# Kernel optimization log

Hardware: AMD Instinct MI355X
Metric: run time of the kernel (lower is better)

## Reference

```python
import jax, jax.numpy as jnp
import numpy as np

B, N, M = 1024, 1024, 64


def setup_inputs() -> dict:
    key = jax.random.key(0)
    ks = jax.random.split(key, 9)
    return {
        "memory": jax.random.normal(ks[0], (B, N, M), dtype=jnp.float32),
        "k": jax.random.normal(ks[1], (B, M), dtype=jnp.float32),
        "beta": jax.random.uniform(ks[2], (B, 1), dtype=jnp.float32),
        "g": jax.random.uniform(ks[3], (B, 1), dtype=jnp.float32),
        "s": jax.random.uniform(ks[4], (B, 3), dtype=jnp.float32),
        "gamma": jax.random.uniform(ks[5], (B, 1), dtype=jnp.float32),
        "w_prev": jax.random.uniform(ks[6], (B, N), dtype=jnp.float32),
        "e": jax.random.uniform(ks[7], (B, M), dtype=jnp.float32),
        "a": jax.random.normal(ks[8], (B, M), dtype=jnp.float32),
    }


def reference(memory, k, beta, g, s, gamma, w_prev, e, a):
    EPS = 1e-16
    COS_EPS = 1e-8  # torch cosine_similarity norm clamp

    # --- _similarity: content addressing (cosine sim + softmax over N) ---
    mem_e = memory + EPS                      # (B, N, M)
    k_e = (k + EPS)[:, None, :]               # (B, 1, M)
    dot = jnp.sum(mem_e * k_e, axis=-1)       # (B, N)
    denom = (jnp.maximum(jnp.linalg.norm(mem_e, axis=-1), COS_EPS)
             * jnp.maximum(jnp.linalg.norm(k_e, axis=-1), COS_EPS))
    wc = jax.nn.softmax(beta * (dot / denom), axis=1)  # (B, N)

    # --- _interpolate ---
    wg = g * wc + (1.0 - g) * w_prev           # (B, N)

    # --- _shift: 3-tap circular convolution, vectorized over batch ---
    # c[i] = s[0]*w[i-1] + s[1]*w[i] + s[2]*w[i+1]  (circular)
    w_hat = (s[:, 0:1] * jnp.roll(wg, 1, axis=1)
             + s[:, 1:2] * wg
             + s[:, 2:3] * jnp.roll(wg, -1, axis=1))

    # --- _sharpen ---
    w = w_hat ** gamma
    w = w / (jnp.sum(w, axis=1, keepdims=True) + EPS)  # (B, N)

    # --- read ---
    read = jnp.einsum('bn,bnm->bm', w, memory)         # (B, M)

    # --- write: rank-1 erase / add ---
    erase = w[:, :, None] * e[:, None, :]              # (B, N, M)
    add = w[:, :, None] * a[:, None, :]                # (B, N, M)
    new_mem = memory * (1.0 - erase) + add             # (B, N, M)

    # pack read (as an extra row) with the updated memory: (B, N+1, M)
    return jnp.concatenate([read[:, None, :], new_mem], axis=1)
```

## Files before the change

### kernel.cpp

```cpp
#include <hip/hip_runtime.h>
#include <cmath>

#define NB 1024
#define NN 1024
#define MM 64
#define NT 512
#define NW (NT / 64)
#define ITS (NN / 32)

typedef float f32x4 __attribute__((ext_vector_type(4)));

__device__ __forceinline__ float block_sum(float v, float* s_tmp) {
    #pragma unroll
    for (int off = 32; off > 0; off >>= 1) v += __shfl_xor(v, off, 64);
    if ((threadIdx.x & 63) == 0) s_tmp[threadIdx.x >> 6] = v;
    __syncthreads();
    float r = 0.0f;
    #pragma unroll
    for (int i = 0; i < NW; ++i) r += s_tmp[i];
    __syncthreads();
    return r;
}

__device__ __forceinline__ float block_max(float v, float* s_tmp) {
    #pragma unroll
    for (int off = 32; off > 0; off >>= 1) v = fmaxf(v, __shfl_xor(v, off, 64));
    if ((threadIdx.x & 63) == 0) s_tmp[threadIdx.x >> 6] = v;
    __syncthreads();
    float r = s_tmp[0];
    #pragma unroll
    for (int i = 1; i < NW; ++i) r = fmaxf(r, s_tmp[i]);
    __syncthreads();
    return r;
}

__global__ void __launch_bounds__(NT, 2) ntm_fused(
    const float* __restrict__ memory,
    const float* __restrict__ k,
    const float* __restrict__ beta,
    const float* __restrict__ g,
    const float* __restrict__ s,
    const float* __restrict__ gamma,
    const float* __restrict__ w_prev,
    const float* __restrict__ e,
    const float* __restrict__ a,
    float* __restrict__ out)
{
    __shared__ float  s_sc[NN];
    __shared__ float  s_w[NN];
    __shared__ float  s_k[MM];
    __shared__ float  s_tmp[NW];
    __shared__ f32x4  s_red[NW * 16];

    const int t  = threadIdx.x;
    const int cg = t & 15;
    const int rg = t >> 4;
    const int b  = blockIdx.x;

    const float* memb = memory + (size_t)b * NN * MM;
    float*       outb = out    + (size_t)b * (NN + 1) * MM;

    const float bet = beta[b], gb = g[b];
    const float s0 = s[b * 3 + 0], s1 = s[b * 3 + 1], s2 = s[b * 3 + 2];
    const float gam = gamma[b];
    const float wp0 = w_prev[(size_t)b * NN + t];
    const float wp1 = w_prev[(size_t)b * NN + t + 512];
    const f32x4 e4 = *(const f32x4*)(e + b * MM + 4 * cg);
    const f32x4 a4 = *(const f32x4*)(a + b * MM + 4 * cg);

    f32x4 mc[ITS];
    #pragma unroll
    for (int it = 0; it < ITS; ++it) {
        int n = it * 32 + rg;
        mc[it] = __builtin_nontemporal_load(
            (const f32x4*)(memb + (size_t)n * MM + 4 * cg));
    }

    if (t < MM) s_k[t] = k[b * MM + t] + 1e-16f;
    float kq = (t < MM) ? s_k[t] * s_k[t] : 0.0f;
    float kden = fmaxf(sqrtf(block_sum(kq, s_tmp)), 1e-8f);
    const f32x4 k4 = ((const f32x4*)s_k)[cg];

    #pragma unroll
    for (int it = 0; it < ITS; ++it) {
        int n = it * 32 + rg;
        f32x4 m4 = mc[it];
        float ex = m4.x + 1e-16f, ey = m4.y + 1e-16f;
        float ez = m4.z + 1e-16f, ew = m4.w + 1e-16f;
        float d = ex * k4.x + ey * k4.y + ez * k4.z + ew * k4.w;
        float q = ex * ex + ey * ey + ez * ez + ew * ew;
        #pragma unroll
        for (int off = 8; off > 0; off >>= 1) {
            d += __shfl_xor(d, off, 64);
            q += __shfl_xor(q, off, 64);
        }
        if (cg == 0) s_sc[n] = bet * d / (fmaxf(sqrtf(q), 1e-8f) * kden);
    }
    __syncthreads();

    float sc0 = s_sc[t], sc1 = s_sc[t + 512];
    float mx = block_max(fmaxf(sc0, sc1), s_tmp);
    float e0 = __expf(sc0 - mx), e1 = __expf(sc1 - mx);
    float inv = 1.0f / block_sum(e0 + e1, s_tmp);

    const float omg = 1.0f - gb;
    s_sc[t]       = gb * e0 * inv + omg * wp0;
    s_sc[t + 512] = gb * e1 * inv + omg * wp1;
    __syncthreads();

    float wv0, wv1;
    {
        int nm = (t == 0) ? NN - 1 : t - 1;
        wv0 = powf(s0 * s_sc[nm] + s1 * s_sc[t] + s2 * s_sc[t + 1], gam);
    }
    {
        int n = t + 512;
        int np = (n == NN - 1) ? 0 : n + 1;
        wv1 = powf(s0 * s_sc[n - 1] + s1 * s_sc[n] + s2 * s_sc[np], gam);
    }
    float winv = 1.0f / (block_sum(wv0 + wv1, s_tmp) + 1e-16f);
    s_w[t]       = wv0 * winv;
    s_w[t + 512] = wv1 * winv;
    __syncthreads();

    f32x4 acc = {0.f, 0.f, 0.f, 0.f};
    #pragma unroll
    for (int it = 0; it < ITS; ++it) {
        int n = it * 32 + rg;
        f32x4 m4 = mc[it];
        float wn = s_w[n];
        acc.x += wn * m4.x; acc.y += wn * m4.y;
        acc.z += wn * m4.z; acc.w += wn * m4.w;
        f32x4 o;
        o.x = m4.x * (1.0f - wn * e4.x) + wn * a4.x;
        o.y = m4.y * (1.0f - wn * e4.y) + wn * a4.y;
        o.z = m4.z * (1.0f - wn * e4.z) + wn * a4.z;
        o.w = m4.w * (1.0f - wn * e4.w) + wn * a4.w;
        __builtin_nontemporal_store(o, (f32x4*)(outb + (size_t)(n + 1) * MM + 4 * cg));
    }

    const int wid = t >> 6, lane = t & 63;
    #pragma unroll
    for (int off = 16; off <= 32; off <<= 1) {
        acc.x += __shfl_xor(acc.x, off, 64);
        acc.y += __shfl_xor(acc.y, off, 64);
        acc.z += __shfl_xor(acc.z, off, 64);
        acc.w += __shfl_xor(acc.w, off, 64);
    }
    if (lane < 16) s_red[wid * 16 + lane] = acc;
    __syncthreads();
    if (t < 16) {
        f32x4 r = {0.f, 0.f, 0.f, 0.f};
        #pragma unroll
        for (int wv = 0; wv < NW; ++wv) {
            f32x4 v = s_red[wv * 16 + t];
            r.x += v.x; r.y += v.y; r.z += v.z; r.w += v.w;
        }
        __builtin_nontemporal_store(r, (f32x4*)(outb + 4 * t));
    }
}

extern "C" void kernel_launch(void* const* d_in, const int* in_sizes, int n_in,
                              void* d_out, int out_size, void* d_ws, size_t ws_size,
                              hipStream_t stream) {
    ntm_fused<<<NB, NT, 0, stream>>>(
        (const float*)d_in[0],
        (const float*)d_in[1],
        (const float*)d_in[2],
        (const float*)d_in[3],
        (const float*)d_in[4],
        (const float*)d_in[5],
        (const float*)d_in[6],
        (const float*)d_in[7],
        (const float*)d_in[8],
        (float*)d_out);
}
```

Baseline: 471.5 us.

## Make kernel persistent over batches with register prefetch of next memory tile

Launches 256 blocks that each process four batch items in sequence. While the current item's updated memory is being stored, the next item's memory slice is loaded into the same registers. The intent is to hide load latency behind the write phase and cut per-block launch overhead. In exchange, fewer blocks are resident, so there is less cross-block overlap during the serial softmax and sharpen reductions.

```diff
diff --git a/kernel.cpp b/kernel.cpp
--- a/kernel.cpp
+++ b/kernel.cpp
@@ -1,12 +1,14 @@
 #include <hip/hip_runtime.h>
 #include <cmath>
 
-#define NB 1024
-#define NN 1024
-#define MM 64
-#define NT 512
-#define NW (NT / 64)
-#define ITS (NN / 32)
+#define NB   1024
+#define NN   1024
+#define MM   64
+#define NT   512
+#define NW   (NT / 64)
+#define ITS  (NN / 32)
+#define GRID 256
+#define BPB  (NB / GRID)
 
 typedef float f32x4 __attribute__((ext_vector_type(4)));
 
@@ -52,118 +54,130 @@
     __shared__ float  s_tmp[NW];
     __shared__ f32x4  s_red[NW * 16];
 
-    const int t  = threadIdx.x;
-    const int cg = t & 15;
-    const int rg = t >> 4;
-    const int b  = blockIdx.x;
-
-    const float* memb = memory + (size_t)b * NN * MM;
-    float*       outb = out    + (size_t)b * (NN + 1) * MM;
-
-    const float bet = beta[b], gb = g[b];
-    const float s0 = s[b * 3 + 0], s1 = s[b * 3 + 1], s2 = s[b * 3 + 2];
-    const float gam = gamma[b];
-    const float wp0 = w_prev[(size_t)b * NN + t];
-    const float wp1 = w_prev[(size_t)b * NN + t + 512];
-    const f32x4 e4 = *(const f32x4*)(e + b * MM + 4 * cg);
-    const f32x4 a4 = *(const f32x4*)(a + b * MM + 4 * cg);
+    const int t    = threadIdx.x;
+    const int cg   = t & 15;
+    const int rg   = t >> 4;
+    const int wid  = t >> 6;
+    const int lane = t & 63;
+    const int coff = 4 * cg;
 
     f32x4 mc[ITS];
-    #pragma unroll
-    for (int it = 0; it < ITS; ++it) {
-        int n = it * 32 + rg;
-        mc[it] = __builtin_nontemporal_load(
-            (const f32x4*)(memb + (size_t)n * MM + 4 * cg));
+    const int bbase = blockIdx.x * BPB;
+
+    {
+        const float* memb = memory + (size_t)bbase * NN * MM;
+        #pragma unroll
+        for (int it = 0; it < ITS; ++it)
+            mc[it] = __builtin_nontemporal_load(
+                (const f32x4*)(memb + (size_t)(it * 32 + rg) * MM + coff));
     }
 
-    if (t < MM) s_k[t] = k[b * MM + t] + 1e-16f;
-    float kq = (t < MM) ? s_k[t] * s_k[t] : 0.0f;
-    float kden = fmaxf(sqrtf(block_sum(kq, s_tmp)), 1e-8f);
-    const f32x4 k4 = ((const f32x4*)s_k)[cg];
+    for (int bi = 0; bi < BPB; ++bi) {
+        const int  b  = bbase + bi;
+        const bool pf = (bi + 1 < BPB);
+        const float* membn = memory + (size_t)(b + 1) * NN * MM;
+        float*       outb  = out    + (size_t)b * (NN + 1) * MM;
 
-    #pragma unroll
-    for (int it = 0; it < ITS; ++it) {
-        int n = it * 32 + rg;
-        f32x4 m4 = mc[it];
-        float ex = m4.x + 1e-16f, ey = m4.y + 1e-16f;
-        float ez = m4.z + 1e-16f, ew = m4.w + 1e-16f;
-        float d = ex * k4.x + ey * k4.y + ez * k4.z + ew * k4.w;
-        float q = ex * ex + ey * ey + ez * ez + ew * ew;
+        const float bet = beta[b], gb = g[b];
+        const float s0 = s[b * 3 + 0], s1 = s[b * 3 + 1], s2 = s[b * 3 + 2];
+        const float gam = gamma[b];
+        const float wp0 = w_prev[(size_t)b * NN + t];
+        const float wp1 = w_prev[(size_t)b * NN + t + 512];
+        const f32x4 e4 = *(const f32x4*)(e + b * MM + coff);
+        const f32x4 a4 = *(const f32x4*)(a + b * MM + coff);
+
+        if (t < MM) s_k[t] = k[b * MM + t] + 1e-16f;
+        float kq = (t < MM) ? s_k[t] * s_k[t] : 0.0f;
+        float kden = fmaxf(sqrtf(block_sum(kq, s_tmp)), 1e-8f);
+        const f32x4 k4 = ((const f32x4*)s_k)[cg];
+
         #pragma unroll
-        for (int off = 8; off > 0; off >>= 1) {
-            d += __shfl_xor(d, off, 64);
-            q += __shfl_xor(q, off, 64);
+        for (int it = 0; it < ITS; ++it) {
+            int n = it * 32 + rg;
+            f32x4 m4 = mc[it];
+            float ex = m4.x + 1e-16f, ey = m4.y + 1e-16f;
+            float ez = m4.z + 1e-16f, ew = m4.w + 1e-16f;
+            float d = ex * k4.x + ey * k4.y + ez * k4.z + ew * k4.w;
+            float q = ex * ex + ey * ey + ez * ez + ew * ew;
+            #pragma unroll
+            for (int off = 8; off > 0; off >>= 1) {
+                d += __shfl_xor(d, off, 64);
+                q += __shfl_xor(q, off, 64);
+            }
+            if (cg == 0) s_sc[n] = bet * d / (fmaxf(sqrtf(q), 1e-8f) * kden);
         }
-        if (cg == 0) s_sc[n] = bet * d / (fmaxf(sqrtf(q), 1e-8f) * kden);
-    }
-    __syncthreads();
+        __syncthreads();
 
-    float sc0 = s_sc[t], sc1 = s_sc[t + 512];
-    float mx = block_max(fmaxf(sc0, sc1), s_tmp);
-    float e0 = __expf(sc0 - mx), e1 = __expf(sc1 - mx);
-    float inv = 1.0f / block_sum(e0 + e1, s_tmp);
+        float sc0 = s_sc[t], sc1 = s_sc[t + 512];
+        float mx = block_max(fmaxf(sc0, sc1), s_tmp);
+        float e0 = __expf(sc0 - mx), e1 = __expf(sc1 - mx);
+        float inv = 1.0f / block_sum(e0 + e1, s_tmp);
 
-    const float omg = 1.0f - gb;
-    s_sc[t]       = gb * e0 * inv + omg * wp0;
-    s_sc[t + 512] = gb * e1 * inv + omg * wp1;
-    __syncthreads();
+        const float omg = 1.0f - gb;
+        s_sc[t]       = gb * e0 * inv + omg * wp0;
+        s_sc[t + 512] = gb * e1 * inv + omg * wp1;
+        __syncthreads();
 
-    float wv0, wv1;
-    {
-        int nm = (t == 0) ? NN - 1 : t - 1;
-        wv0 = powf(s0 * s_sc[nm] + s1 * s_sc[t] + s2 * s_sc[t + 1], gam);
-    }
-    {
-        int n = t + 512;
-        int np = (n == NN - 1) ? 0 : n + 1;
-        wv1 = powf(s0 * s_sc[n - 1] + s1 * s_sc[n] + s2 * s_sc[np], gam);
-    }
-    float winv = 1.0f / (block_sum(wv0 + wv1, s_tmp) + 1e-16f);
-    s_w[t]       = wv0 * winv;
-    s_w[t + 512] = wv1 * winv;
-    __syncthreads();
+        float wv0, wv1;
+        {
+            int nm = (t == 0) ? NN - 1 : t - 1;
+            wv0 = powf(s0 * s_sc[nm] + s1 * s_sc[t] + s2 * s_sc[t + 1], gam);
+        }
+        {
+            int n = t + 512;
+            int np = (n == NN - 1) ? 0 : n + 1;
+            wv1 = powf(s0 * s_sc[n - 1] + s1 * s_sc[n] + s2 * s_sc[np], gam);
+        }
+        float winv = 1.0f / (block_sum(wv0 + wv1, s_tmp) + 1e-16f);
+        s_w[t]       = wv0 * winv;
+        s_w[t + 512] = wv1 * winv;
+        __syncthreads();
 
-    f32x4 acc = {0.f, 0.f, 0.f, 0.f};
-    #pragma unroll
-    for (int it = 0; it < ITS; ++it) {
-        int n = it * 32 + rg;
-        f32x4 m4 = mc[it];
-        float wn = s_w[n];
-        acc.x += wn * m4.x; acc.y += wn * m4.y;
-        acc.z += wn * m4.z; acc.w += wn * m4.w;
-        f32x4 o;
-        o.x = m4.x * (1.0f - wn * e4.x) + wn * a4.x;
-        o.y = m4.y * (1.0f - wn * e4.y) + wn * a4.y;
-        o.z = m4.z * (1.0f - wn * e4.z) + wn * a4.z;
-        o.w = m4.w * (1.0f - wn * e4.w) + wn * a4.w;
-        __builtin_nontemporal_store(o, (f32x4*)(outb + (size_t)(n + 1) * MM + 4 * cg));
-    }
+        f32x4 acc = {0.f, 0.f, 0.f, 0.f};
+        #pragma unroll
+        for (int it = 0; it < ITS; ++it) {
+            int n = it * 32 + rg;
+            f32x4 m4 = mc[it];
+            float wn = s_w[n];
+            acc.x += wn * m4.x; acc.y += wn * m4.y;
+            acc.z += wn * m4.z; acc.w += wn * m4.w;
+            f32x4 o;
+            o.x = m4.x * (1.0f - wn * e4.x) + wn * a4.x;
+            o.y = m4.y * (1.0f - wn * e4.y) + wn * a4.y;
+            o.z = m4.z * (1.0f - wn * e4.z) + wn * a4.z;
+            o.w = m4.w * (1.0f - wn * e4.w) + wn * a4.w;
+            __builtin_nontemporal_store(o, (f32x4*)(outb + (size_t)(n + 1) * MM + coff));
+            if (pf)
+                mc[it] = __builtin_nontemporal_load(
+                    (const f32x4*)(membn + (size_t)n * MM + coff));
+        }
 
-    const int wid = t >> 6, lane = t & 63;
-    #pragma unroll
-    for (int off = 16; off <= 32; off <<= 1) {
-        acc.x += __shfl_xor(acc.x, off, 64);
-        acc.y += __shfl_xor(acc.y, off, 64);
-        acc.z += __shfl_xor(acc.z, off, 64);
-        acc.w += __shfl_xor(acc.w, off, 64);
-    }
-    if (lane < 16) s_red[wid * 16 + lane] = acc;
-    __syncthreads();
-    if (t < 16) {
-        f32x4 r = {0.f, 0.f, 0.f, 0.f};
         #pragma unroll
-        for (int wv = 0; wv < NW; ++wv) {
-            f32x4 v = s_red[wv * 16 + t];
-            r.x += v.x; r.y += v.y; r.z += v.z; r.w += v.w;
+        for (int off = 16; off <= 32; off <<= 1) {
+            acc.x += __shfl_xor(acc.x, off, 64);
+            acc.y += __shfl_xor(acc.y, off, 64);
+            acc.z += __shfl_xor(acc.z, off, 64);
+            acc.w += __shfl_xor(acc.w, off, 64);
         }
-        __builtin_nontemporal_store(r, (f32x4*)(outb + 4 * t));
+        if (lane < 16) s_red[wid * 16 + lane] = acc;
+        __syncthreads();
+        if (t < 16) {
+            f32x4 r = {0.f, 0.f, 0.f, 0.f};
+            #pragma unroll
+            for (int wv = 0; wv < NW; ++wv) {
+                f32x4 v = s_red[wv * 16 + t];
+                r.x += v.x; r.y += v.y; r.z += v.z; r.w += v.w;
+            }
+            __builtin_nontemporal_store(r, (f32x4*)(outb + 4 * t));
+        }
+        __syncthreads();
     }
 }
 
 extern "C" void kernel_launch(void* const* d_in, const int* in_sizes, int n_in,
                               void* d_out, int out_size, void* d_ws, size_t ws_size,
                               hipStream_t stream) {
-    ntm_fused<<<NB, NT, 0, stream>>>(
+    ntm_fused<<<GRID, NT, 0, stream>>>(
         (const float*)d_in[0],
         (const float*)d_in[1],
         (const float*)d_in[2],
```

New measurement: 586.4 us. 1.24x slower.
